# Optimization experiments

Hardware: AMD Instinct MI355X
Metric: run time of the kernel (lower is better)

## Reference

```python
import jax, jax.numpy as jnp
import numpy as np

CAMS, HEADS, PTS, LAYERS = 6, 8, 2, 3
D, DH, FFN = 256, 32, 512
VZ, VH, VW = 8, 50, 50
NQ = VZ * VH * VW
IN_C = 768
IMG_H, IMG_W = 256, 704
FH, FW = IMG_H // 32, IMG_W // 32   # 8, 22
L = FH * FW                         # 176 tokens per camera
LVIS = 44                           # visible tokens (mask_ratio=0.75)


def _layer_norm(x, g, b, eps=1e-5):
    m = x.mean(-1, keepdims=True)
    v = x.var(-1, keepdims=True)
    return (x - m) / jnp.sqrt(v + eps) * g + b


def _group_norm(x, g, b, groups=16, eps=1e-5):
    B, C = x.shape[0], x.shape[1]
    xg = x.reshape(B, groups, C // groups, *x.shape[2:])
    m = xg.mean(axis=(2, 3, 4, 5), keepdims=True)
    v = xg.var(axis=(2, 3, 4, 5), keepdims=True)
    xg = (xg - m) / jnp.sqrt(v + eps)
    return xg.reshape(x.shape) * g[None, :, None, None, None] + b[None, :, None, None, None]


def _bilinear(val, loc, Hf, Wf):
    # val: [C, HW, heads, dh]; loc: [C, NQ, heads, P, 2] as (x, y) pixel coords
    x, y = loc[..., 0], loc[..., 1]
    x0 = jnp.floor(x); y0 = jnp.floor(y)
    wx, wy = x - x0, y - y0
    x0i, y0i = x0.astype(jnp.int32), y0.astype(jnp.int32)
    cidx = jnp.arange(val.shape[0])[:, None, None, None]
    hidx = jnp.arange(val.shape[2])[None, None, :, None]

    def g(yi, xi):
        idx = jnp.clip(yi, 0, Hf - 1) * Wf + jnp.clip(xi, 0, Wf - 1)
        return val[cidx, idx, hidx]  # [C,NQ,heads,P,dh]

    out = ((1 - wx) * (1 - wy))[..., None] * g(y0i, x0i)
    out = out + (wx * (1 - wy))[..., None] * g(y0i, x0i + 1)
    out = out + ((1 - wx) * wy)[..., None] * g(y0i + 1, x0i)
    out = out + (wx * wy)[..., None] * g(y0i + 1, x0i + 1)
    return out


def setup_inputs() -> dict:
    key = jax.random.key(0)
    ks = iter(jax.random.split(key, 48))

    def rn(shape, s=0.02):
        return jax.random.normal(next(ks), shape, jnp.float32) * s

    return {
        'camera_x': jax.random.normal(next(ks), (CAMS, LVIS, IN_C), jnp.float32),
        'camera_ids_restore': jax.random.randint(next(ks), (CAMS, L), 0, L),
        'img_h': IMG_H, 'img_w': IMG_W,
        'mask_token': rn((1, 1, IN_C)),
        'vol_emb': rn((NQ, D), 1.0),
        'W_tc': rn((D, IN_C)), 'b_tc': jnp.zeros((D,), jnp.float32),
        'cams_embeds': rn((CAMS, D), 1.0),
        'level_embeds': rn((1, D), 1.0),
        'W_off': rn((LAYERS, D, HEADS * CAMS * PTS * 2)),
        'b_off': rn((LAYERS, HEADS * CAMS * PTS * 2), 2.0),
        'W_att': rn((LAYERS, D, HEADS * CAMS * PTS)),
        'b_att': jnp.zeros((LAYERS, HEADS * CAMS * PTS), jnp.float32),
        'W_val': rn((LAYERS, D, D)), 'b_val': jnp.zeros((LAYERS, D), jnp.float32),
        'W_out': rn((LAYERS, D, D)), 'b_out': jnp.zeros((LAYERS, D), jnp.float32),
        'ln1_g': jnp.ones((LAYERS, D), jnp.float32), 'ln1_b': jnp.zeros((LAYERS, D), jnp.float32),
        'W_ff1': rn((LAYERS, D, FFN)), 'b_ff1': jnp.zeros((LAYERS, FFN), jnp.float32),
        'W_ff2': rn((LAYERS, FFN, D)), 'b_ff2': jnp.zeros((LAYERS, D), jnp.float32),
        'ln2_g': jnp.ones((LAYERS, D), jnp.float32), 'ln2_b': jnp.zeros((LAYERS, D), jnp.float32),
        'deconv_w': rn((D, D, 2, 2, 2)),
        'gn1_g': jnp.ones((D,), jnp.float32), 'gn1_b': jnp.zeros((D,), jnp.float32),
        'conv3_w': rn((192, D, 3, 3, 3)),
        'gn2_g': jnp.ones((192,), jnp.float32), 'gn2_b': jnp.zeros((192,), jnp.float32),
    }


def _forward(camera_x, camera_ids_restore, img_h, img_w, mask_token, vol_emb, W_tc, b_tc,
             cams_embeds, level_embeds, W_off, b_off, W_att, b_att, W_val, b_val, W_out, b_out,
             ln1_g, ln1_b, W_ff1, b_ff1, W_ff2, b_ff2, ln2_g, ln2_b,
             deconv_w, gn1_g, gn1_b, conv3_w, gn2_g, gn2_b):
    N, Lfull = camera_ids_restore.shape
    # 1) MAE unshuffle: append mask tokens, gather back to original order
    mt = jnp.broadcast_to(mask_token, (N, Lfull - camera_x.shape[1], IN_C)).astype(camera_x.dtype)
    full = jnp.concatenate([camera_x, mt], axis=1)                         # [N,L,C]
    full = jnp.take_along_axis(full, camera_ids_restore[:, :, None], axis=1)
    Hf, Wf = img_h // 32, img_w // 32
    cam_x = jnp.transpose(full, (0, 2, 1)).reshape(1, N, IN_C, Hf, Wf)     # [1,6,768,8,22]
    # 2) 1x1 transfer conv + ReLU
    vf = jax.nn.relu(jnp.einsum('bnchw,oc->bnohw', cam_x, W_tc) + b_tc[None, None, :, None, None])
    # 3) flatten spatial + cam/level embeds -> per-camera feature maps [N,HW,D]
    vf = jnp.transpose(vf.reshape(1, N, D, Hf * Wf), (1, 0, 3, 2))          # [N,1,HW,D]
    vf = vf + cams_embeds[:, None, None, :] + level_embeds[None, None, 0:1, :]
    feat = vf[:, 0]                                                         # [N,HW,D]
    # 4) reference points of volume queries (z slow, h, w fast) -> pixel coords
    ww = (jnp.arange(VW, dtype=jnp.float32) + 0.5) / VW
    hh = (jnp.arange(VH, dtype=jnp.float32) + 0.5) / VH
    grid = jnp.stack([jnp.tile(ww, VH), jnp.repeat(hh, VW)], axis=-1)       # [VH*VW,2]
    ref_pix = jnp.tile(grid, (VZ, 1)) * jnp.array([Wf, Hf], jnp.float32) - 0.5  # [NQ,2]
    # 5) deformable cross-attention volume encoder
    q = vol_emb
    for l in range(LAYERS):
        off = (q @ W_off[l] + b_off[l]).reshape(NQ, HEADS, CAMS, PTS, 2)
        att = jax.nn.softmax((q @ W_att[l] + b_att[l]).reshape(NQ, HEADS, CAMS * PTS), axis=-1)
        att = jnp.transpose(att.reshape(NQ, HEADS, CAMS, PTS), (2, 0, 1, 3))      # [C,NQ,H,P]
        val = (feat @ W_val[l] + b_val[l]).reshape(CAMS, Hf * Wf, HEADS, DH)
        loc = jnp.transpose(ref_pix[:, None, None, None, :] + off, (2, 0, 1, 3, 4))  # [C,NQ,H,P,2]
        sampled = _bilinear(val, loc, Hf, Wf)                                     # [C,NQ,H,P,DH]
        agg = jnp.einsum('cnhp,cnhpd->nhd', att, sampled).reshape(NQ, D)
        q = _layer_norm(q + agg @ W_out[l] + b_out[l], ln1_g[l], ln1_b[l])
        q = _layer_norm(q + jax.nn.relu(q @ W_ff1[l] + b_ff1[l]) @ W_ff2[l] + b_ff2[l], ln2_g[l], ln2_b[l])
    # 6) reshape -> [1, D, VW, VH, VZ] (matches .permute(0,4,3,2,1))
    vol = jnp.transpose(q.reshape(1, VZ, VH, VW, D), (0, 4, 3, 2, 1))
    # 7) deblock: deconv3d(k=2,s=2) -> GN16 -> ReLU -> conv3d(k=3,p=1) -> GN16 -> ReLU
    x = jax.lax.conv_transpose(vol, deconv_w, (2, 2, 2), 'VALID',
                               dimension_numbers=('NCDHW', 'OIDHW', 'NCDHW'))
    x = jax.nn.relu(_group_norm(x, gn1_g, gn1_b))
    x = jax.lax.conv_general_dilated(x, conv3_w, (1, 1, 1), [(1, 1)] * 3,
                                     dimension_numbers=('NCDHW', 'OIDHW', 'NCDHW'))
    x = jax.nn.relu(_group_norm(x, gn2_g, gn2_b))
    return x, cam_x


def reference(camera_x, camera_ids_restore, img_h, img_w, mask_token, vol_emb, W_tc, b_tc,
              cams_embeds, level_embeds, W_off, b_off, W_att, b_att, W_val, b_val, W_out, b_out,
              ln1_g, ln1_b, W_ff1, b_ff1, W_ff2, b_ff2, ln2_g, ln2_b,
              deconv_w, gn1_g, gn1_b, conv3_w, gn2_g, gn2_b):
    return _forward(camera_x, camera_ids_restore, img_h, img_w, mask_token, vol_emb, W_tc, b_tc,
                    cams_embeds, level_embeds, W_off, b_off, W_att, b_att, W_val, b_val, W_out, b_out,
                    ln1_g, ln1_b, W_ff1, b_ff1, W_ff2, b_ff2, ln2_g, ln2_b,
                    deconv_w, gn1_g, gn1_b, conv3_w, gn2_g, gn2_b)
```

## Files before the change

### kernel.cpp

```cpp
#include <hip/hip_runtime.h>
#include <stdint.h>

typedef __attribute__((ext_vector_type(8))) short s16x8;
typedef __attribute__((ext_vector_type(4))) float f32x4;

static __device__ __forceinline__ unsigned short f2bf(float f) {
  unsigned u = __float_as_uint(f);
  u += 0x7FFFu + ((u >> 16) & 1u);
  return (unsigned short)(u >> 16);
}
static __device__ __forceinline__ float bf2f(unsigned short h) {
  return __uint_as_float(((unsigned)h) << 16);
}
static __device__ __forceinline__ void sum8(uint4 u, float& a, float& q) {
  unsigned w[4] = {u.x, u.y, u.z, u.w};
#pragma unroll
  for (int i = 0; i < 4; ++i) {
    float v0 = __uint_as_float((w[i] & 0xFFFFu) << 16);
    float v1 = __uint_as_float(w[i] & 0xFFFF0000u);
    a += v0 + v1;
    q += v0 * v0 + v1 * v1;
  }
}

__global__ void k_wt(const float* __restrict__ in, unsigned short* __restrict__ out,
                     int K, int N, int outL, int total) {
  int idx = blockIdx.x * 256 + threadIdx.x;
  if (idx >= total) return;
  int kn = K * N;
  int l = idx / kn, r = idx - l * kn;
  int k = r / N, n = r - k * N;
  out[(size_t)l * outL + (size_t)n * K + k] = f2bf(in[idx]);
}

__global__ void k_wdc(const float* __restrict__ in, unsigned short* __restrict__ out) {
  int idx = blockIdx.x * 256 + threadIdx.x;
  int n = idx >> 8, k = idx & 255;
  out[idx] = f2bf(in[((size_t)(n & 255)) * 2048 + k * 8 + (n >> 8)]);
}

__global__ void k_wc3(const float* __restrict__ W, unsigned short* __restrict__ T) {
  int idx = blockIdx.x * 256 + threadIdx.x;
  int tap = idx / 49152;
  int rem = idx - tap * 49152;
  int oc = rem >> 8, ic = rem & 255;
  int chunk = ic >> 5, kg = (ic >> 3) & 3, j = ic & 7;
  int ocblk = oc >> 4, lo = oc & 15;
  size_t frag = (size_t)(tap * 8 + chunk) * 12 + ocblk;
  T[(frag * 64 + kg * 16 + lo) * 8 + j] = f2bf(W[(oc * 256 + ic) * 27 + tap]);
}

__global__ void k_cvt(const float* __restrict__ in, unsigned short* __restrict__ out, int n) {
  int i = blockIdx.x * 256 + threadIdx.x;
  if (i < n) out[i] = f2bf(in[i]);
}

__global__ void k_wtct(const float* __restrict__ W, float* __restrict__ T) {
  int idx = blockIdx.x * 256 + threadIdx.x;
  int k = idx >> 8, o = idx & 255;
  T[idx] = W[o * 768 + k];
}

__global__ void k_restore(const float* __restrict__ cx, const int* __restrict__ ids,
                          const float* __restrict__ mtok, float* __restrict__ out) {
  int idx = blockIdx.x * 256 + threadIdx.x;
  int p = idx % 176;
  int r = idx / 176;
  int ch = r % 768;
  int c = r / 768;
  int id = ids[c * 176 + p];
  out[idx] = (id < 44) ? cx[((size_t)(c * 44 + id)) * 768 + ch] : mtok[ch];
}

__global__ __launch_bounds__(256) void k_vf(const float* __restrict__ camx, const float* __restrict__ WtT,
                                            const float* __restrict__ btc, const float* __restrict__ cemb,
                                            const float* __restrict__ lemb, unsigned short* __restrict__ featb) {
  __shared__ float sa[768];
  int blk = blockIdx.x;
  int c = blk / 176, p = blk - c * 176;
  int t = threadIdx.x;
  for (int i = t; i < 768; i += 256) sa[i] = camx[((size_t)(c * 768 + i)) * 176 + p];
  __syncthreads();
  float acc = 0.f;
  for (int k = 0; k < 768; ++k) acc += sa[k] * WtT[k * 256 + t];
  featb[(size_t)blk * 256 + t] = f2bf(fmaxf(acc + btc[t], 0.f) + cemb[c * 256 + t] + lemb[t]);
}

__global__ __launch_bounds__(256) void k_gemm(
    const unsigned short* __restrict__ A, int M, int lda,
    const unsigned short* __restrict__ Bt, int K, int N,
    const float* __restrict__ bias, const float* __restrict__ bias2, int n1, int relu,
    float* __restrict__ Cf, unsigned short* __restrict__ Cb, int ldc, int mode) {
  __shared__ short sA[128 * 40];
  const int t = threadIdx.x;
  const int l = t & 63, w = t >> 6;
  const int lo = l & 15, kg = l >> 4;
  const int row0 = blockIdx.x * 128, n0 = blockIdx.y * 64;
  const s16x8 bz = {0, 0, 0, 0, 0, 0, 0, 0};
  f32x4 acc[2][4] = {};
  s16x8 bc[4], bn[4];
#pragma unroll
  for (int nb = 0; nb < 4; ++nb) {
    int n = n0 + nb * 16 + lo;
    bc[nb] = (n < N) ? *(const s16x8*)&Bt[(size_t)n * K + kg * 8] : bz;
  }
  const int stR = t >> 1, stH = t & 1;
  for (int kc = 0; kc < K; kc += 32) {
    const bool pf = (kc + 32 < K);
    if (pf) {
#pragma unroll
      for (int nb = 0; nb < 4; ++nb) {
        int n = n0 + nb * 16 + lo;
        bn[nb] = (n < N) ? *(const s16x8*)&Bt[(size_t)n * K + kc + 32 + kg * 8] : bz;
      }
    }
    __syncthreads();
    {
      int r = row0 + stR;
// ... 21 lines not shown
  }
#pragma unroll
  for (int m = 0; m < 2; ++m)
#pragma unroll
    for (int nb = 0; nb < 4; ++nb)
#pragma unroll
      for (int r = 0; r < 4; ++r) {
        int row = row0 + w * 32 + m * 16 + (kg << 2) + r;
        int col = n0 + nb * 16 + lo;
        if (row < M && col < N) {
          float v = acc[m][nb][r];
          if (bias) v += (col < n1) ? bias[col] : bias2[col - n1];
          if (relu) v = fmaxf(v, 0.f);
          if (mode == 0) {
            Cf[(size_t)row * ldc + col] = v;
          } else if (mode == 2) {
            Cb[(size_t)row * ldc + col] = f2bf(v);
          } else {
            int tap = col >> 8, oc = col & 255;
            int z = row / 2500, rr = row - z * 2500;
            int hy = rr / 50, wx = rr - hy * 50;
            int t1 = tap >> 2, t2 = (tap >> 1) & 1, t3 = tap & 1;
            int od = 2 * wx + 1 - t1, oh = 2 * hy + 1 - t2, ow = 2 * z + 1 - t3;
            Cb[((size_t)((od * 100 + oh) * 16 + ow)) * 256 + oc] = f2bf(v);
          }
        }
      }
}

__global__ __launch_bounds__(256) void k_sample(const float* __restrict__ oa,
                                                const float* __restrict__ val,
                                                unsigned short* __restrict__ aggb) {
  __shared__ float sl[96], sw[96];
  int n = blockIdx.x, t = threadIdx.x;
  if (t < 96) sl[t] = oa[(size_t)n * 288 + 192 + t];
  __syncthreads();
  if (t < 8) {
    float mx = -1e30f;
    for (int j = 0; j < 12; ++j) mx = fmaxf(mx, sl[t * 12 + j]);
    float s = 0.f;
    for (int j = 0; j < 12; ++j) s += __expf(sl[t * 12 + j] - mx);
    float inv = 1.f / s;
    for (int j = 0; j < 12; ++j) sw[t * 12 + j] = __expf(sl[t * 12 + j] - mx) * inv;
  }
  __syncthreads();
  int h = t >> 5, d = t & 31;
  float xr = ((float)(n % 50) + 0.5f) * (22.0f / 50.0f) - 0.5f;
  float yr = ((float)((n / 50) % 50) + 0.5f) * (8.0f / 50.0f) - 0.5f;
  float acc = 0.f;
  const float* offn = oa + (size_t)n * 288 + h * 24;
  const float* vbh = val + (size_t)h * 32 + d;
#pragma unroll
  for (int c = 0; c < 6; ++c)
#pragma unroll
    for (int p2 = 0; p2 < 2; ++p2) {
      float x = xr + offn[(c * 2 + p2) * 2];
      float y = yr + offn[(c * 2 + p2) * 2 + 1];
      float x0 = floorf(x), y0 = floorf(y);
      float wx = x - x0, wy = y - y0;
      int ix0 = min(max((int)x0, 0), 21), ix1 = min(max((int)x0 + 1, 0), 21);
      int iy0 = min(max((int)y0, 0), 7), iy1 = min(max((int)y0 + 1, 0), 7);
      const float* vb = vbh + (size_t)c * 176 * 256;
      float v00 = vb[(size_t)(iy0 * 22 + ix0) * 256];
      float v01 = vb[(size_t)(iy0 * 22 + ix1) * 256];
      float v10 = vb[(size_t)(iy1 * 22 + ix0) * 256];
      float v11 = vb[(size_t)(iy1 * 22 + ix1) * 256];
      float bil = (1.f - wx) * (1.f - wy) * v00 + wx * (1.f - wy) * v01 +
                  (1.f - wx) * wy * v10 + wx * wy * v11;
      acc += sw[h * 12 + c * 2 + p2] * bil;
    }
  aggb[(size_t)n * 256 + t] = f2bf(acc);
}

__global__ __launch_bounds__(256) void k_addln(float* __restrict__ q, const float* __restrict__ p,
                                               const float* __restrict__ g, const float* __restrict__ b,
                                               unsigned short* __restrict__ qb) {
  __shared__ float red[8];
  int n = blockIdx.x, t = threadIdx.x;
  float x = q[(size_t)n * 256 + t] + p[(size_t)n * 256 + t];
  float s1 = x, s2 = x * x;
#pragma unroll
  for (int o = 32; o >= 1; o >>= 1) {
    s1 += __shfl_xor(s1, o, 64);
    s2 += __shfl_xor(s2, o, 64);
  }
  int w = t >> 6;
  if ((t & 63) == 0) { red[w * 2] = s1; red[w * 2 + 1] = s2; }
  __syncthreads();
  s1 = red[0] + red[2] + red[4] + red[6];
  s2 = red[1] + red[3] + red[5] + red[7];
  float mean = s1 * (1.0f / 256.0f);
  float var = s2 * (1.0f / 256.0f) - mean * mean;
  float y = (x - mean) * rsqrtf(var + 1e-5f) * g[t] + b[t];
  q[(size_t)n * 256 + t] = y;
  qb[(size_t)n * 256 + t] = f2bf(y);
}

__global__ __launch_bounds__(256) void k_gnstat1(const unsigned short* __restrict__ X, float* __restrict__ part) {
  __shared__ float s1[256], s2[256];
  int b = blockIdx.x, t = threadIdx.x;
  int oc8 = t & 31, v0 = t >> 5;
  float a = 0.f, q = 0.f;
#pragma unroll
  for (int i = 0; i < 8; ++i) {
    int vox = v0 + i * 8;
    uint4 u = *(const uint4*)&X[(size_t)b * 16384 + vox * 256 + oc8 * 8];
    sum8(u, a, q);
  }
  s1[t] = a; s2[t] = q;
  __syncthreads();
  if (t < 128) { s1[t] += s1[t + 128]; s2[t] += s2[t + 128]; }
  __syncthreads();
  if (t < 64) { s1[t] += s1[t + 64]; s2[t] += s2[t + 64]; }
  __syncthreads();
  if (t < 32) { s1[t] += s1[t + 32]; s2[t] += s2[t + 32]; }
  __syncthreads();
  if (t < 16) {
    part[t * 2500 + b] = s1[2 * t] + s1[2 * t + 1];
    part[40000 + t * 2500 + b] = s2[2 * t] + s2[2 * t + 1];
  }
}

__global__ __launch_bounds__(256) void k_gnred1(const float* __restrict__ part, float* __restrict__ gmv) {
  __shared__ float s1[256], s2[256];
  int g = blockIdx.x, t = threadIdx.x;
  float a = 0.f, q = 0.f;
  for (int i = t; i < 2500; i += 256) { a += part[g * 2500 + i]; q += part[40000 + g * 2500 + i]; }
  s1[t] = a; s2[t] = q;
  __syncthreads();
  for (int s = 128; s > 0; s >>= 1) {
    if (t < s) { s1[t] += s1[t + s]; s2[t] += s2[t + s]; }
    __syncthreads();
  }
  if (t == 0) {
    float m = s1[0] / 2560000.0f;
    float v = s2[0] / 2560000.0f - m * m;
    gmv[2 * g] = m; gmv[2 * g + 1] = rsqrtf(v + 1e-5f);
  }
}

__global__ __launch_bounds__(256) void k_gnapply1(unsigned short* __restrict__ X, const float* __restrict__ gmv,
                                                  const float* __restrict__ g, const float* __restrict__ b) {
  for (unsigned i = blockIdx.x * 256 + threadIdx.x; i < 5120000u; i += gridDim.x * 256) {
    unsigned e = i * 8u;
    int oc0 = e & 255, grp = oc0 >> 4;
    float mean = gmv[grp * 2], rstd = gmv[grp * 2 + 1];
    float4 g0 = *(const float4*)&g[oc0], g1 = *(const float4*)&g[oc0 + 4];
    float4 b0 = *(const float4*)&b[oc0], b1 = *(const float4*)&b[oc0 + 4];
    uint4 u = *(const uint4*)&X[e];
    unsigned w[4] = {u.x, u.y, u.z, u.w};
    float gg[8] = {g0.x, g0.y, g0.z, g0.w, g1.x, g1.y, g1.z, g1.w};
    float bb[8] = {b0.x, b0.y, b0.z, b0.w, b1.x, b1.y, b1.z, b1.w};
    unsigned o[4];
#pragma unroll
    for (int j = 0; j < 4; ++j) {
      float v0 = __uint_as_float((w[j] & 0xFFFFu) << 16);
      float v1 = __uint_as_float(w[j] & 0xFFFF0000u);
      v0 = fmaxf((v0 - mean) * rstd * gg[2 * j] + bb[2 * j], 0.f);
      v1 = fmaxf((v1 - mean) * rstd * gg[2 * j + 1] + bb[2 * j + 1], 0.f);
      o[j] = (unsigned)f2bf(v0) | ((unsigned)f2bf(v1) << 16);
    }
    *(uint4*)&X[e] = make_uint4(o[0], o[1], o[2], o[3]);
  }
}

__global__ __launch_bounds__(256, 2) void k_conv3(const unsigned short* __restrict__ X,
                                                  const unsigned short* __restrict__ Wp,
                                                  unsigned short* __restrict__ Y) {
  __shared__ short sX[4 * 543 * 8];
  int bid = blockIdx.x;
  int xcd = bid & 7, idx = bid >> 3;
  int swz = (xcd < 4 ? xcd * 163 : 652 + (xcd - 4) * 162) + idx;
  const int od = swz / 13;
  const int oh0 = (swz - od * 13) * 8;
  const int t = threadIdx.x;
  const int l = t & 63, w = t >> 6;
  const int kg = l >> 4, lo = l & 15;
  f32x4 acc[8][3] = {};
  s16x8 bc[9], bn[9];
  const unsigned short* Wl = Wp + (size_t)l * 8;
  const int w3 = w * 3;
#pragma unroll
  for (int t2 = 0; t2 < 3; ++t2)
#pragma unroll
    for (int nb = 0; nb < 3; ++nb)
      bc[t2 * 3 + nb] = *(const s16x8*)&Wl[(size_t)((t2 * 3 * 8) * 12 + w3 + nb) * 512];

  for (int g = 0; g < 72; ++g) {
    const int chunk = g / 9;
    const int sub = g - chunk * 9;
    const int t1 = sub / 3, t3 = sub - t1 * 3;
    if (sub == 0) {
      __syncthreads();
#pragma unroll
      for (int i = 0; i < 9; ++i) {
        int e = t + i * 256;
        if (e < 2160) {
          int pos = e >> 2, ks = e & 3;
          int sd = pos / 180, r2 = pos - sd * 180;
          int sh = r2 / 18, sw_ = r2 - sh * 18;
          int gd = od + sd - 1, gh = oh0 + sh - 1, gw = sw_ - 1;
          uint4 v = {0u, 0u, 0u, 0u};
          if ((unsigned)gd < 100u && (unsigned)gh < 100u && (unsigned)gw < 16u)
            v = *(const uint4*)&X[((size_t)((gd * 100 + gh) * 16 + gw)) * 256 + chunk * 32 + ks * 8];
          *(uint4*)&sX[(ks * 543 + pos) * 8] = v;
        }
      }
      __syncthreads();
    }
    const int g1 = g + 1;
    if (g1 < 72) {
      const int c1 = g1 / 9, s1 = g1 - c1 * 9;
      const int t1n = s1 / 3, t3n = s1 - t1n * 3;
#pragma unroll
      for (int t2 = 0; t2 < 3; ++t2)
#pragma unroll
        for (int nb = 0; nb < 3; ++nb)
          bn[t2 * 3 + nb] = *(const s16x8*)&Wl[
              (size_t)(((t1n * 9 + t2 * 3 + t3n) * 8 + c1) * 12 + w3 + nb) * 512];
    }
    const int abase = kg * 543 + t1 * 180 + lo + t3;
#pragma unroll
    for (int sh = 0; sh < 10; ++sh) {
      s16x8 a = *(const s16x8*)&sX[(abase + sh * 18) * 8];
#pragma unroll
      for (int t2 = 0; t2 < 3; ++t2) {
        const int m = sh - t2;
        if (m >= 0 && m < 8) {
          acc[m][0] = __builtin_amdgcn_mfma_f32_16x16x32_bf16(a, bc[t2 * 3 + 0], acc[m][0], 0, 0, 0);
          acc[m][1] = __builtin_amdgcn_mfma_f32_16x16x32_bf16(a, bc[t2 * 3 + 1], acc[m][1], 0, 0, 0);
          acc[m][2] = __builtin_amdgcn_mfma_f32_16x16x32_bf16(a, bc[t2 * 3 + 2], acc[m][2], 0, 0, 0);
        }
      }
    }
#pragma unroll
    for (int i = 0; i < 9; ++i) bc[i] = bn[i];
  }
#pragma unroll
  for (int m = 0; m < 8; ++m) {
    int oh = oh0 + m;
    if (oh < 100) {
#pragma unroll
      for (int nb = 0; nb < 3; ++nb)
#pragma unroll
        for (int r = 0; r < 4; ++r) {
          int oc = w * 48 + nb * 16 + lo;
          int ow = (kg << 2) + r;
          Y[(size_t)oc * 160000 + (size_t)((od * 100 + oh) * 16) + ow] = f2bf(acc[m][nb][r]);
        }
    }
  }
}

__global__ __launch_bounds__(256) void k_gnstat2(const unsigned short* __restrict__ X, float* __restrict__ part) {
  __shared__ float s1[256], s2[256];
  int b = blockIdx.x, t = threadIdx.x;
  int ch = b / 10, pp = b - ch * 10;
  const unsigned short* base = X + (size_t)ch * 160000 + (size_t)pp * 16000;
  float a = 0.f, q = 0.f;
  for (int i = t; i < 2000; i += 256) {
    uint4 u = *(const uint4*)&base[i * 8];
    sum8(u, a, q);
  }
  s1[t] = a; s2[t] = q;
  __syncthreads();
  for (int s = 128; s > 0; s >>= 1) {
    if (t < s) { s1[t] += s1[t + s]; s2[t] += s2[t + s]; }
    __syncthreads();
  }
  if (t == 0) { part[80000 + ch * 10 + pp] = s1[0]; part[81920 + ch * 10 + pp] = s2[0]; }
}

__global__ __launch_bounds__(256) void k_gnred2(const float* __restrict__ part, float* __restrict__ gmv) {
  __shared__ float s1[256], s2[256];
  int g = blockIdx.x, t = threadIdx.x;
  float a = (t < 120) ? part[80000 + g * 120 + t] : 0.f;
  float q = (t < 120) ? part[81920 + g * 120 + t] : 0.f;
  s1[t] = a; s2[t] = q;
  __syncthreads();
// ... 59 lines not shown
  const float* b_ff1 = (const float*)d_in[21];
  const float* W_ff2 = (const float*)d_in[22];
  const float* b_ff2 = (const float*)d_in[23];
  const float* ln2_g = (const float*)d_in[24];
  const float* ln2_b = (const float*)d_in[25];
  const float* deconv_w = (const float*)d_in[26];
  const float* gn1_g = (const float*)d_in[27];
  const float* gn1_b = (const float*)d_in[28];
  const float* conv3_w = (const float*)d_in[29];
  const float* gn2_g = (const float*)d_in[30];
  const float* gn2_b = (const float*)d_in[31];

  char* ws = (char*)d_ws;
  float* q             = (float*)(ws + 0);
  unsigned short* qb   = (unsigned short*)(ws + 20480000);
  float* proj          = (float*)(ws + 30720000);
  float* oa            = (float*)(ws + 51200000);
  unsigned short* aggb = (unsigned short*)(ws + 74240000);
  unsigned short* ffhb = (unsigned short*)(ws + 84480000);
  float* val           = (float*)(ws + 104960000);
  unsigned short* featb= (unsigned short*)(ws + 106041344);
  unsigned short* x1bf = (unsigned short*)(ws + 30720000);
  unsigned short* c3   = (unsigned short*)(ws + 112640000);
  unsigned short* Wt_val = (unsigned short*)(ws + 174080000);
  unsigned short* Wt_oa  = (unsigned short*)(ws + 174473216);
  unsigned short* Wt_out = (unsigned short*)(ws + 174915584);
  unsigned short* Wt_ff1 = (unsigned short*)(ws + 175308800);
  unsigned short* Wt_ff2 = (unsigned short*)(ws + 176095232);
  unsigned short* Wt_dc  = (unsigned short*)(ws + 176881664);
  unsigned short* wc3    = (unsigned short*)(ws + 177930240);
  float* part = (float*)(ws + 180584448);
  float* gmv1 = (float*)(ws + 180920320);
  float* gmv2 = (float*)(ws + 180920448);
  float* wtcT = (float*)(ws + 180920576);

  float* out_x = (float*)d_out;
  float* out_camx = out_x + 30720000;

  k_wtct<<<768, 256, 0, stream>>>(W_tc, wtcT);
  k_wt<<<(3 * 65536 + 255) / 256, 256, 0, stream>>>(W_val, Wt_val, 256, 256, 65536, 3 * 65536);
  k_wt<<<(3 * 49152 + 255) / 256, 256, 0, stream>>>(W_off, Wt_oa, 256, 192, 73728, 3 * 49152);
  k_wt<<<(3 * 24576 + 255) / 256, 256, 0, stream>>>(W_att, Wt_oa + 192 * 256, 256, 96, 73728, 3 * 24576);
  k_wt<<<(3 * 65536 + 255) / 256, 256, 0, stream>>>(W_out, Wt_out, 256, 256, 65536, 3 * 65536);
  k_wt<<<(3 * 131072 + 255) / 256, 256, 0, stream>>>(W_ff1, Wt_ff1, 256, 512, 131072, 3 * 131072);
  k_wt<<<(3 * 131072 + 255) / 256, 256, 0, stream>>>(W_ff2, Wt_ff2, 512, 256, 131072, 3 * 131072);
  k_wdc<<<2048, 256, 0, stream>>>(deconv_w, Wt_dc);
  k_wc3<<<5184, 256, 0, stream>>>(conv3_w, wc3);

  k_restore<<<3168, 256, 0, stream>>>(camera_x, ids, mask_tok, out_camx);
  k_vf<<<1056, 256, 0, stream>>>(out_camx, wtcT, b_tc, cams_emb, lvl_emb, featb);
  hipMemcpyAsync(q, vol_emb, (size_t)20000 * 256 * 4, hipMemcpyDeviceToDevice, stream);
  k_cvt<<<20000, 256, 0, stream>>>(vol_emb, qb, 5120000);

  for (int lyr = 0; lyr < 3; ++lyr) {
    k_gemm<<<gemm_grid(1056, 256), 256, 0, stream>>>(featb, 1056, 256, Wt_val + lyr * 65536, 256, 256,
                                                     b_val + lyr * 256, nullptr, 256, 0, val, nullptr, 256, 0);
    k_gemm<<<gemm_grid(20000, 288), 256, 0, stream>>>(qb, 20000, 256, Wt_oa + lyr * 73728, 256, 288,
                                                      b_off + lyr * 192, b_att + lyr * 96, 192, 0,
                                                      oa, nullptr, 288, 0);
    k_sample<<<20000, 256, 0, stream>>>(oa, val, aggb);
    k_gemm<<<gemm_grid(20000, 256), 256, 0, stream>>>(aggb, 20000, 256, Wt_out + lyr * 65536, 256, 256,
                                                      b_out + lyr * 256, nullptr, 256, 0, proj, nullptr, 256, 0);
    k_addln<<<20000, 256, 0, stream>>>(q, proj, ln1_g + lyr * 256, ln1_b + lyr * 256, qb);
    k_gemm<<<gemm_grid(20000, 512), 256, 0, stream>>>(qb, 20000, 256, Wt_ff1 + lyr * 131072, 256, 512,
                                                      b_ff1 + lyr * 512, nullptr, 512, 1, nullptr, ffhb, 512, 2);
    k_gemm<<<gemm_grid(20000, 256), 256, 0, stream>>>(ffhb, 20000, 512, Wt_ff2 + lyr * 131072, 512, 256,
                                                      b_ff2 + lyr * 256, nullptr, 256, 0, proj, nullptr, 256, 0);
    k_addln<<<20000, 256, 0, stream>>>(q, proj, ln2_g + lyr * 256, ln2_b + lyr * 256, qb);
  }

  k_gemm<<<gemm_grid(20000, 2048), 256, 0, stream>>>(qb, 20000, 256, Wt_dc, 256, 2048,
                                                     nullptr, nullptr, 2048, 0, nullptr, x1bf, 256, 1);

  k_gnstat1<<<2500, 256, 0, stream>>>(x1bf, part);
  k_gnred1<<<16, 256, 0, stream>>>(part, gmv1);
  k_gnapply1<<<2048, 256, 0, stream>>>(x1bf, gmv1, gn1_g, gn1_b);

  k_conv3<<<1300, 256, 0, stream>>>(x1bf, wc3, c3);

  k_gnstat2<<<1920, 256, 0, stream>>>(c3, part);
  k_gnred2<<<16, 256, 0, stream>>>(part, gmv2);
  k_gnapply2<<<2048, 256, 0, stream>>>(c3, gmv2, gn2_g, gn2_b, out_x);
}
```

Measured before the change: 1.353 ms.

## Fuse GroupNorm1 apply into conv3 load, rebalance conv3 waves, batch rows in sample/addln

The GN1 normalize+ReLU pass is folded into the conv3 shared-memory staging, using per-channel scale and shift precomputed by a tiny kernel. This removes one full read-modify-write pass over the 80 MB bf16 volume. conv3 moves from 4 to 6 waves per block, each owning 32 output channels instead of 48, with fewer live registers, occupancy hint 3, and s_setprio around the MFMA loop. k_sample and k_addln each process 8 rows per block to cut launch and block overhead, at the cost of extra barriers and less parallelism per block.

```diff
diff --git a/kernel.cpp b/kernel.cpp
--- a/kernel.cpp
+++ b/kernel.cpp
@@ -171,68 +171,77 @@
                                                 const float* __restrict__ val,
                                                 unsigned short* __restrict__ aggb) {
   __shared__ float sl[96], sw[96];
-  int n = blockIdx.x, t = threadIdx.x;
-  if (t < 96) sl[t] = oa[(size_t)n * 288 + 192 + t];
-  __syncthreads();
-  if (t < 8) {
-    float mx = -1e30f;
-    for (int j = 0; j < 12; ++j) mx = fmaxf(mx, sl[t * 12 + j]);
-    float s = 0.f;
-    for (int j = 0; j < 12; ++j) s += __expf(sl[t * 12 + j] - mx);
-    float inv = 1.f / s;
-    for (int j = 0; j < 12; ++j) sw[t * 12 + j] = __expf(sl[t * 12 + j] - mx) * inv;
-  }
-  __syncthreads();
+  int t = threadIdx.x;
   int h = t >> 5, d = t & 31;
-  float xr = ((float)(n % 50) + 0.5f) * (22.0f / 50.0f) - 0.5f;
-  float yr = ((float)((n / 50) % 50) + 0.5f) * (8.0f / 50.0f) - 0.5f;
-  float acc = 0.f;
-  const float* offn = oa + (size_t)n * 288 + h * 24;
-  const float* vbh = val + (size_t)h * 32 + d;
-#pragma unroll
-  for (int c = 0; c < 6; ++c)
-#pragma unroll
-    for (int p2 = 0; p2 < 2; ++p2) {
-      float x = xr + offn[(c * 2 + p2) * 2];
-      float y = yr + offn[(c * 2 + p2) * 2 + 1];
-      float x0 = floorf(x), y0 = floorf(y);
-      float wx = x - x0, wy = y - y0;
-      int ix0 = min(max((int)x0, 0), 21), ix1 = min(max((int)x0 + 1, 0), 21);
-      int iy0 = min(max((int)y0, 0), 7), iy1 = min(max((int)y0 + 1, 0), 7);
-      const float* vb = vbh + (size_t)c * 176 * 256;
-      float v00 = vb[(size_t)(iy0 * 22 + ix0) * 256];
-      float v01 = vb[(size_t)(iy0 * 22 + ix1) * 256];
-      float v10 = vb[(size_t)(iy1 * 22 + ix0) * 256];
-      float v11 = vb[(size_t)(iy1 * 22 + ix1) * 256];
-      float bil = (1.f - wx) * (1.f - wy) * v00 + wx * (1.f - wy) * v01 +
-                  (1.f - wx) * wy * v10 + wx * wy * v11;
-      acc += sw[h * 12 + c * 2 + p2] * bil;
-    }
-  aggb[(size_t)n * 256 + t] = f2bf(acc);
+  const float* vbh0 = val + (size_t)h * 32 + d;
+  for (int r = 0; r < 8; ++r) {
+    int n = blockIdx.x * 8 + r;
+    if (t < 96) sl[t] = oa[(size_t)n * 288 + 192 + t];
+    __syncthreads();
+    if (t < 8) {
+      float mx = -1e30f;
+      for (int j = 0; j < 12; ++j) mx = fmaxf(mx, sl[t * 12 + j]);
+      float s = 0.f;
+      for (int j = 0; j < 12; ++j) s += __expf(sl[t * 12 + j] - mx);
+      float inv = 1.f / s;
+      for (int j = 0; j < 12; ++j) sw[t * 12 + j] = __expf(sl[t * 12 + j] - mx) * inv;
+    }
+    __syncthreads();
+    float xr = ((float)(n % 50) + 0.5f) * (22.0f / 50.0f) - 0.5f;
+    float yr = ((float)((n / 50) % 50) + 0.5f) * (8.0f / 50.0f) - 0.5f;
+    float acc = 0.f;
+    const float* offn = oa + (size_t)n * 288 + h * 24;
+#pragma unroll
+    for (int c = 0; c < 6; ++c)
+#pragma unroll
+      for (int p2 = 0; p2 < 2; ++p2) {
+        float x = xr + offn[(c * 2 + p2) * 2];
+        float y = yr + offn[(c * 2 + p2) * 2 + 1];
+        float x0 = floorf(x), y0 = floorf(y);
+        float wx = x - x0, wy = y - y0;
+        int ix0 = min(max((int)x0, 0), 21), ix1 = min(max((int)x0 + 1, 0), 21);
+        int iy0 = min(max((int)y0, 0), 7), iy1 = min(max((int)y0 + 1, 0), 7);
+        const float* vb = vbh0 + (size_t)c * 176 * 256;
+        float v00 = vb[(size_t)(iy0 * 22 + ix0) * 256];
+        float v01 = vb[(size_t)(iy0 * 22 + ix1) * 256];
+        float v10 = vb[(size_t)(iy1 * 22 + ix0) * 256];
+        float v11 = vb[(size_t)(iy1 * 22 + ix1) * 256];
+        float bil = (1.f - wx) * (1.f - wy) * v00 + wx * (1.f - wy) * v01 +
+                    (1.f - wx) * wy * v10 + wx * wy * v11;
+        acc += sw[h * 12 + c * 2 + p2] * bil;
+      }
+    aggb[(size_t)n * 256 + t] = f2bf(acc);
+    __syncthreads();
+  }
 }
 
 __global__ __launch_bounds__(256) void k_addln(float* __restrict__ q, const float* __restrict__ p,
                                                const float* __restrict__ g, const float* __restrict__ b,
                                                unsigned short* __restrict__ qb) {
   __shared__ float red[8];
-  int n = blockIdx.x, t = threadIdx.x;
-  float x = q[(size_t)n * 256 + t] + p[(size_t)n * 256 + t];
-  float s1 = x, s2 = x * x;
-#pragma unroll
-  for (int o = 32; o >= 1; o >>= 1) {
-    s1 += __shfl_xor(s1, o, 64);
-    s2 += __shfl_xor(s2, o, 64);
-  }
+  int t = threadIdx.x;
   int w = t >> 6;
-  if ((t & 63) == 0) { red[w * 2] = s1; red[w * 2 + 1] = s2; }
-  __syncthreads();
-  s1 = red[0] + red[2] + red[4] + red[6];
-  s2 = red[1] + red[3] + red[5] + red[7];
-  float mean = s1 * (1.0f / 256.0f);
-  float var = s2 * (1.0f / 256.0f) - mean * mean;
-  float y = (x - mean) * rsqrtf(var + 1e-5f) * g[t] + b[t];
-  q[(size_t)n * 256 + t] = y;
-  qb[(size_t)n * 256 + t] = f2bf(y);
+  float gg = g[t], bb = b[t];
+  for (int r = 0; r < 8; ++r) {
+    size_t n = (size_t)blockIdx.x * 8 + r;
+    float x = q[n * 256 + t] + p[n * 256 + t];
+    float s1 = x, s2 = x * x;
+#pragma unroll
+    for (int o = 32; o >= 1; o >>= 1) {
+      s1 += __shfl_xor(s1, o, 64);
+      s2 += __shfl_xor(s2, o, 64);
+    }
+    if ((t & 63) == 0) { red[w * 2] = s1; red[w * 2 + 1] = s2; }
+    __syncthreads();
+    s1 = red[0] + red[2] + red[4] + red[6];
+    s2 = red[1] + red[3] + red[5] + red[7];
+    float mean = s1 * (1.0f / 256.0f);
+    float var = s2 * (1.0f / 256.0f) - mean * mean;
+    float y = (x - mean) * rsqrtf(var + 1e-5f) * gg + bb;
+    q[n * 256 + t] = y;
+    qb[n * 256 + t] = f2bf(y);
+    __syncthreads();
+  }
 }
 
 __global__ __launch_bounds__(256) void k_gnstat1(const unsigned short* __restrict__ X, float* __restrict__ part) {
@@ -278,33 +287,19 @@
   }
 }
 
-__global__ __launch_bounds__(256) void k_gnapply1(unsigned short* __restrict__ X, const float* __restrict__ gmv,
-                                                  const float* __restrict__ g, const float* __restrict__ b) {
-  for (unsigned i = blockIdx.x * 256 + threadIdx.x; i < 5120000u; i += gridDim.x * 256) {
-    unsigned e = i * 8u;
-    int oc0 = e & 255, grp = oc0 >> 4;
-    float mean = gmv[grp * 2], rstd = gmv[grp * 2 + 1];
-    float4 g0 = *(const float4*)&g[oc0], g1 = *(const float4*)&g[oc0 + 4];
-    float4 b0 = *(const float4*)&b[oc0], b1 = *(const float4*)&b[oc0 + 4];
-    uint4 u = *(const uint4*)&X[e];
-    unsigned w[4] = {u.x, u.y, u.z, u.w};
-    float gg[8] = {g0.x, g0.y, g0.z, g0.w, g1.x, g1.y, g1.z, g1.w};
-    float bb[8] = {b0.x, b0.y, b0.z, b0.w, b1.x, b1.y, b1.z, b1.w};
-    unsigned o[4];
-#pragma unroll
-    for (int j = 0; j < 4; ++j) {
-      float v0 = __uint_as_float((w[j] & 0xFFFFu) << 16);
-      float v1 = __uint_as_float(w[j] & 0xFFFF0000u);
-      v0 = fmaxf((v0 - mean) * rstd * gg[2 * j] + bb[2 * j], 0.f);
-      v1 = fmaxf((v1 - mean) * rstd * gg[2 * j + 1] + bb[2 * j + 1], 0.f);
-      o[j] = (unsigned)f2bf(v0) | ((unsigned)f2bf(v1) << 16);
-    }
-    *(uint4*)&X[e] = make_uint4(o[0], o[1], o[2], o[3]);
-  }
-}
-
-__global__ __launch_bounds__(256, 2) void k_conv3(const unsigned short* __restrict__ X,
+__global__ void k_gnscale(const float* __restrict__ gmv, const float* __restrict__ g,
+                          const float* __restrict__ b, float* __restrict__ sct) {
+  int t = threadIdx.x;
+  int grp = t >> 4;
+  float mean = gmv[2 * grp], rstd = gmv[2 * grp + 1];
+  float s = rstd * g[t];
+  sct[t] = s;
+  sct[256 + t] = b[t] - mean * s;
+}
+
+__global__ __launch_bounds__(384, 3) void k_conv3(const unsigned short* __restrict__ X,
                                                   const unsigned short* __restrict__ Wp,
+                                                  const float* __restrict__ sct,
                                                   unsigned short* __restrict__ Y) {
   __shared__ short sX[4 * 543 * 8];
   int bid = blockIdx.x;
@@ -315,50 +310,70 @@
   const int t = threadIdx.x;
   const int l = t & 63, w = t >> 6;
   const int kg = l >> 4, lo = l & 15;
-  f32x4 acc[8][3] = {};
-  s16x8 bc[9], bn[9];
+  f32x4 acc[8][2] = {};
+  s16x8 bc[6], bn[6];
   const unsigned short* Wl = Wp + (size_t)l * 8;
-  const int w3 = w * 3;
+  const int w2 = w * 2;
 #pragma unroll
   for (int t2 = 0; t2 < 3; ++t2)
 #pragma unroll
-    for (int nb = 0; nb < 3; ++nb)
-      bc[t2 * 3 + nb] = *(const s16x8*)&Wl[(size_t)((t2 * 3 * 8) * 12 + w3 + nb) * 512];
-
-  for (int g = 0; g < 72; ++g) {
-    const int chunk = g / 9;
-    const int sub = g - chunk * 9;
+    for (int nb = 0; nb < 2; ++nb)
+      bc[t2 * 2 + nb] = *(const s16x8*)&Wl[(size_t)((t2 * 3 * 8) * 12 + w2 + nb) * 512];
+
+  for (int gi = 0; gi < 72; ++gi) {
+    const int chunk = gi / 9;
+    const int sub = gi - chunk * 9;
     const int t1 = sub / 3, t3 = sub - t1 * 3;
     if (sub == 0) {
       __syncthreads();
 #pragma unroll
-      for (int i = 0; i < 9; ++i) {
-        int e = t + i * 256;
+      for (int i = 0; i < 6; ++i) {
+        int e = t + i * 384;
         if (e < 2160) {
           int pos = e >> 2, ks = e & 3;
           int sd = pos / 180, r2 = pos - sd * 180;
           int sh = r2 / 18, sw_ = r2 - sh * 18;
           int gd = od + sd - 1, gh = oh0 + sh - 1, gw = sw_ - 1;
           uint4 v = {0u, 0u, 0u, 0u};
-          if ((unsigned)gd < 100u && (unsigned)gh < 100u && (unsigned)gw < 16u)
+          if ((unsigned)gd < 100u && (unsigned)gh < 100u && (unsigned)gw < 16u) {
             v = *(const uint4*)&X[((size_t)((gd * 100 + gh) * 16 + gw)) * 256 + chunk * 32 + ks * 8];
+            int ic0 = chunk * 32 + ks * 8;
+            float4 sA0 = *(const float4*)&sct[ic0];
+            float4 sA1 = *(const float4*)&sct[ic0 + 4];
+            float4 tA0 = *(const float4*)&sct[256 + ic0];
+            float4 tA1 = *(const float4*)&sct[256 + ic0 + 4];
+            float sc[8] = {sA0.x, sA0.y, sA0.z, sA0.w, sA1.x, sA1.y, sA1.z, sA1.w};
+            float tt[8] = {tA0.x, tA0.y, tA0.z, tA0.w, tA1.x, tA1.y, tA1.z, tA1.w};
+            unsigned wv[4] = {v.x, v.y, v.z, v.w};
+            unsigned o[4];
+#pragma unroll
+            for (int j = 0; j < 4; ++j) {
+              float v0 = __uint_as_float((wv[j] & 0xFFFFu) << 16);
+              float v1 = __uint_as_float(wv[j] & 0xFFFF0000u);
+              v0 = fmaxf(v0 * sc[2 * j] + tt[2 * j], 0.f);
+              v1 = fmaxf(v1 * sc[2 * j + 1] + tt[2 * j + 1], 0.f);
+              o[j] = (unsigned)f2bf(v0) | ((unsigned)f2bf(v1) << 16);
+            }
+            v = make_uint4(o[0], o[1], o[2], o[3]);
+          }
           *(uint4*)&sX[(ks * 543 + pos) * 8] = v;
         }
       }
       __syncthreads();
     }
-    const int g1 = g + 1;
-    if (g1 < 72) {
-      const int c1 = g1 / 9, s1 = g1 - c1 * 9;
-      const int t1n = s1 / 3, t3n = s1 - t1n * 3;
+    const int gn1 = gi + 1;
+    if (gn1 < 72) {
+      const int c1 = gn1 / 9, su1 = gn1 - c1 * 9;
+      const int t1n = su1 / 3, t3n = su1 - t1n * 3;
 #pragma unroll
       for (int t2 = 0; t2 < 3; ++t2)
 #pragma unroll
-        for (int nb = 0; nb < 3; ++nb)
-          bn[t2 * 3 + nb] = *(const s16x8*)&Wl[
-              (size_t)(((t1n * 9 + t2 * 3 + t3n) * 8 + c1) * 12 + w3 + nb) * 512];
+        for (int nb = 0; nb < 2; ++nb)
+          bn[t2 * 2 + nb] = *(const s16x8*)&Wl[
+              (size_t)(((t1n * 9 + t2 * 3 + t3n) * 8 + c1) * 12 + w2 + nb) * 512];
     }
     const int abase = kg * 543 + t1 * 180 + lo + t3;
+    __builtin_amdgcn_s_setprio(1);
 #pragma unroll
     for (int sh = 0; sh < 10; ++sh) {
       s16x8 a = *(const s16x8*)&sX[(abase + sh * 18) * 8];
@@ -366,24 +381,24 @@
       for (int t2 = 0; t2 < 3; ++t2) {
         const int m = sh - t2;
         if (m >= 0 && m < 8) {
-          acc[m][0] = __builtin_amdgcn_mfma_f32_16x16x32_bf16(a, bc[t2 * 3 + 0], acc[m][0], 0, 0, 0);
-          acc[m][1] = __builtin_amdgcn_mfma_f32_16x16x32_bf16(a, bc[t2 * 3 + 1], acc[m][1], 0, 0, 0);
-          acc[m][2] = __builtin_amdgcn_mfma_f32_16x16x32_bf16(a, bc[t2 * 3 + 2], acc[m][2], 0, 0, 0);
+          acc[m][0] = __builtin_amdgcn_mfma_f32_16x16x32_bf16(a, bc[t2 * 2 + 0], acc[m][0], 0, 0, 0);
+          acc[m][1] = __builtin_amdgcn_mfma_f32_16x16x32_bf16(a, bc[t2 * 2 + 1], acc[m][1], 0, 0, 0);
         }
       }
     }
-#pragma unroll
-    for (int i = 0; i < 9; ++i) bc[i] = bn[i];
+    __builtin_amdgcn_s_setprio(0);
+#pragma unroll
+    for (int i = 0; i < 6; ++i) bc[i] = bn[i];
   }
 #pragma unroll
   for (int m = 0; m < 8; ++m) {
     int oh = oh0 + m;
     if (oh < 100) {
 #pragma unroll
-      for (int nb = 0; nb < 3; ++nb)
+      for (int nb = 0; nb < 2; ++nb)
 #pragma unroll
         for (int r = 0; r < 4; ++r) {
-          int oc = w * 48 + nb * 16 + lo;
+          int oc = w * 32 + nb * 16 + lo;
           int ow = (kg << 2) + r;
           Y[(size_t)oc * 160000 + (size_t)((od * 100 + oh) * 16) + ow] = f2bf(acc[m][nb][r]);
         }
@@ -510,6 +525,7 @@
   float* gmv1 = (float*)(ws + 180920320);
   float* gmv2 = (float*)(ws + 180920448);
   float* wtcT = (float*)(ws + 180920576);
+  float* sct  = (float*)(ws + 181707008);
 
   float* out_x = (float*)d_out;
   float* out_camx = out_x + 30720000;
@@ -535,15 +551,15 @@
     k_gemm<<<gemm_grid(20000, 288), 256, 0, stream>>>(qb, 20000, 256, Wt_oa + lyr * 73728, 256, 288,
                                                       b_off + lyr * 192, b_att + lyr * 96, 192, 0,
                                                       oa, nullptr, 288, 0);
-    k_sample<<<20000, 256, 0, stream>>>(oa, val, aggb);
+    k_sample<<<2500, 256, 0, stream>>>(oa, val, aggb);
     k_gemm<<<gemm_grid(20000, 256), 256, 0, stream>>>(aggb, 20000, 256, Wt_out + lyr * 65536, 256, 256,
                                                       b_out + lyr * 256, nullptr, 256, 0, proj, nullptr, 256, 0);
-    k_addln<<<20000, 256, 0, stream>>>(q, proj, ln1_g + lyr * 256, ln1_b + lyr * 256, qb);
+    k_addln<<<2500, 256, 0, stream>>>(q, proj, ln1_g + lyr * 256, ln1_b + lyr * 256, qb);
     k_gemm<<<gemm_grid(20000, 512), 256, 0, stream>>>(qb, 20000, 256, Wt_ff1 + lyr * 131072, 256, 512,
                                                       b_ff1 + lyr * 512, nullptr, 512, 1, nullptr, ffhb, 512, 2);
     k_gemm<<<gemm_grid(20000, 256), 256, 0, stream>>>(ffhb, 20000, 512, Wt_ff2 + lyr * 131072, 512, 256,
                                                       b_ff2 + lyr * 256, nullptr, 256, 0, proj, nullptr, 256, 0);
-    k_addln<<<20000, 256, 0, stream>>>(q, proj, ln2_g + lyr * 256, ln2_b + lyr * 256, qb);
+    k_addln<<<2500, 256, 0, stream>>>(q, proj, ln2_g + lyr * 256, ln2_b + lyr * 256, qb);
   }
 
   k_gemm<<<gemm_grid(20000, 2048), 256, 0, stream>>>(qb, 20000, 256, Wt_dc, 256, 2048,
@@ -551,9 +567,9 @@
 
   k_gnstat1<<<2500, 256, 0, stream>>>(x1bf, part);
   k_gnred1<<<16, 256, 0, stream>>>(part, gmv1);
-  k_gnapply1<<<2048, 256, 0, stream>>>(x1bf, gmv1, gn1_g, gn1_b);
-
-  k_conv3<<<1300, 256, 0, stream>>>(x1bf, wc3, c3);
+  k_gnscale<<<1, 256, 0, stream>>>(gmv1, gn1_g, gn1_b, sct);
+
+  k_conv3<<<1300, 384, 0, stream>>>(x1bf, wc3, sct, c3);
 
   k_gnstat2<<<1920, 256, 0, stream>>>(c3, part);
   k_gnred2<<<16, 256, 0, stream>>>(part, gmv2);
```

Result: slower. 1.549 ms (+14.5%).

## Route camera projection through MFMA GEMM and batch rows in sample/LN kernels

Applied to the files above, without the earlier changes.

The scalar fp32 camera-token projection kernel is replaced by a bf16 restore-transpose, a call to the existing MFMA GEMM with bias and ReLU, and a separate embedding-add pass. The sampling and add-LayerNorm kernels now process 8 rows per block with 2500 blocks instead of 20000, which cuts launch and block-scheduling overhead. The sampling softmax is also parallelised across 96 threads. The projection input is now bf16 and the embeddings are added after a bf16 rounding, which adds rounding error. Fewer blocks may also reduce the latency hiding available for the gathers.

```diff
diff --git a/kernel.cpp b/kernel.cpp
--- a/kernel.cpp
+++ b/kernel.cpp
@@ -55,12 +55,6 @@
   if (i < n) out[i] = f2bf(in[i]);
 }
 
-__global__ void k_wtct(const float* __restrict__ W, float* __restrict__ T) {
-  int idx = blockIdx.x * 256 + threadIdx.x;
-  int k = idx >> 8, o = idx & 255;
-  T[idx] = W[o * 768 + k];
-}
-
 __global__ void k_restore(const float* __restrict__ cx, const int* __restrict__ ids,
                           const float* __restrict__ mtok, float* __restrict__ out) {
   int idx = blockIdx.x * 256 + threadIdx.x;
@@ -72,18 +66,23 @@
   out[idx] = (id < 44) ? cx[((size_t)(c * 44 + id)) * 768 + ch] : mtok[ch];
 }
 
-__global__ __launch_bounds__(256) void k_vf(const float* __restrict__ camx, const float* __restrict__ WtT,
-                                            const float* __restrict__ btc, const float* __restrict__ cemb,
-                                            const float* __restrict__ lemb, unsigned short* __restrict__ featb) {
-  __shared__ float sa[768];
-  int blk = blockIdx.x;
-  int c = blk / 176, p = blk - c * 176;
-  int t = threadIdx.x;
-  for (int i = t; i < 768; i += 256) sa[i] = camx[((size_t)(c * 768 + i)) * 176 + p];
-  __syncthreads();
-  float acc = 0.f;
-  for (int k = 0; k < 768; ++k) acc += sa[k] * WtT[k * 256 + t];
-  featb[(size_t)blk * 256 + t] = f2bf(fmaxf(acc + btc[t], 0.f) + cemb[c * 256 + t] + lemb[t]);
+__global__ void k_restoreT(const float* __restrict__ cx, const int* __restrict__ ids,
+                           const float* __restrict__ mtok, unsigned short* __restrict__ out) {
+  int idx = blockIdx.x * 256 + threadIdx.x;
+  int ch = idx % 768;
+  int row = idx / 768;
+  int c = row / 176, p = row - c * 176;
+  int id = ids[c * 176 + p];
+  float v = (id < 44) ? cx[((size_t)(c * 44 + id)) * 768 + ch] : mtok[ch];
+  out[idx] = f2bf(v);
+}
+
+__global__ void k_embadd(unsigned short* __restrict__ featb, const float* __restrict__ cemb,
+                         const float* __restrict__ lemb) {
+  int idx = blockIdx.x * 256 + threadIdx.x;
+  int col = idx & 255;
+  int c = idx / (176 * 256);
+  featb[idx] = f2bf(bf2f(featb[idx]) + cemb[c * 256 + col] + lemb[col]);
 }
 
 __global__ __launch_bounds__(256) void k_gemm(
@@ -171,68 +170,80 @@
                                                 const float* __restrict__ val,
                                                 unsigned short* __restrict__ aggb) {
   __shared__ float sl[96], sw[96];
-  int n = blockIdx.x, t = threadIdx.x;
-  if (t < 96) sl[t] = oa[(size_t)n * 288 + 192 + t];
-  __syncthreads();
-  if (t < 8) {
-    float mx = -1e30f;
-    for (int j = 0; j < 12; ++j) mx = fmaxf(mx, sl[t * 12 + j]);
-    float s = 0.f;
-    for (int j = 0; j < 12; ++j) s += __expf(sl[t * 12 + j] - mx);
-    float inv = 1.f / s;
-    for (int j = 0; j < 12; ++j) sw[t * 12 + j] = __expf(sl[t * 12 + j] - mx) * inv;
-  }
-  __syncthreads();
+  int t = threadIdx.x;
   int h = t >> 5, d = t & 31;
-  float xr = ((float)(n % 50) + 0.5f) * (22.0f / 50.0f) - 0.5f;
-  float yr = ((float)((n / 50) % 50) + 0.5f) * (8.0f / 50.0f) - 0.5f;
-  float acc = 0.f;
-  const float* offn = oa + (size_t)n * 288 + h * 24;
-  const float* vbh = val + (size_t)h * 32 + d;
-#pragma unroll
-  for (int c = 0; c < 6; ++c)
-#pragma unroll
-    for (int p2 = 0; p2 < 2; ++p2) {
-      float x = xr + offn[(c * 2 + p2) * 2];
-      float y = yr + offn[(c * 2 + p2) * 2 + 1];
-      float x0 = floorf(x), y0 = floorf(y);
-      float wx = x - x0, wy = y - y0;
-      int ix0 = min(max((int)x0, 0), 21), ix1 = min(max((int)x0 + 1, 0), 21);
-      int iy0 = min(max((int)y0, 0), 7), iy1 = min(max((int)y0 + 1, 0), 7);
-      const float* vb = vbh + (size_t)c * 176 * 256;
-      float v00 = vb[(size_t)(iy0 * 22 + ix0) * 256];
-      float v01 = vb[(size_t)(iy0 * 22 + ix1) * 256];
-      float v10 = vb[(size_t)(iy1 * 22 + ix0) * 256];
-      float v11 = vb[(size_t)(iy1 * 22 + ix1) * 256];
-      float bil = (1.f - wx) * (1.f - wy) * v00 + wx * (1.f - wy) * v01 +
-                  (1.f - wx) * wy * v10 + wx * wy * v11;
-      acc += sw[h * 12 + c * 2 + p2] * bil;
-    }
-  aggb[(size_t)n * 256 + t] = f2bf(acc);
+  const float* vbh0 = val + (size_t)h * 32 + d;
+  for (int r = 0; r < 8; ++r) {
+    int n = blockIdx.x * 8 + r;
+    if (t < 96) sl[t] = oa[(size_t)n * 288 + 192 + t];
+    __syncthreads();
+    if (t < 96) {
+      int hh = t / 12;
+      float mx = -1e30f;
+#pragma unroll
+      for (int j = 0; j < 12; ++j) mx = fmaxf(mx, sl[hh * 12 + j]);
+      sw[t] = __expf(sl[t] - mx);
+    }
+    __syncthreads();
+    float ssum = 0.f;
+#pragma unroll
+    for (int j = 0; j < 12; ++j) ssum += sw[h * 12 + j];
+    float inv = 1.f / ssum;
+    float xr = ((float)(n % 50) + 0.5f) * (22.0f / 50.0f) - 0.5f;
+    float yr = ((float)((n / 50) % 50) + 0.5f) * (8.0f / 50.0f) - 0.5f;
+    float acc = 0.f;
+    const float* offn = oa + (size_t)n * 288 + h * 24;
+#pragma unroll
+    for (int c = 0; c < 6; ++c)
+#pragma unroll
+      for (int p2 = 0; p2 < 2; ++p2) {
+        float x = xr + offn[(c * 2 + p2) * 2];
+        float y = yr + offn[(c * 2 + p2) * 2 + 1];
+        float x0 = floorf(x), y0 = floorf(y);
+        float wx = x - x0, wy = y - y0;
+        int ix0 = min(max((int)x0, 0), 21), ix1 = min(max((int)x0 + 1, 0), 21);
+        int iy0 = min(max((int)y0, 0), 7), iy1 = min(max((int)y0 + 1, 0), 7);
+        const float* vb = vbh0 + (size_t)c * 176 * 256;
+        float v00 = vb[(size_t)(iy0 * 22 + ix0) * 256];
+        float v01 = vb[(size_t)(iy0 * 22 + ix1) * 256];
+        float v10 = vb[(size_t)(iy1 * 22 + ix0) * 256];
+        float v11 = vb[(size_t)(iy1 * 22 + ix1) * 256];
+        float bil = (1.f - wx) * (1.f - wy) * v00 + wx * (1.f - wy) * v01 +
+                    (1.f - wx) * wy * v10 + wx * wy * v11;
+        acc += sw[h * 12 + c * 2 + p2] * inv * bil;
+      }
+    aggb[(size_t)n * 256 + t] = f2bf(acc);
+    __syncthreads();
+  }
 }
 
 __global__ __launch_bounds__(256) void k_addln(float* __restrict__ q, const float* __restrict__ p,
                                                const float* __restrict__ g, const float* __restrict__ b,
                                                unsigned short* __restrict__ qb) {
   __shared__ float red[8];
-  int n = blockIdx.x, t = threadIdx.x;
-  float x = q[(size_t)n * 256 + t] + p[(size_t)n * 256 + t];
-  float s1 = x, s2 = x * x;
-#pragma unroll
-  for (int o = 32; o >= 1; o >>= 1) {
-    s1 += __shfl_xor(s1, o, 64);
-    s2 += __shfl_xor(s2, o, 64);
-  }
+  int t = threadIdx.x;
   int w = t >> 6;
-  if ((t & 63) == 0) { red[w * 2] = s1; red[w * 2 + 1] = s2; }
-  __syncthreads();
-  s1 = red[0] + red[2] + red[4] + red[6];
-  s2 = red[1] + red[3] + red[5] + red[7];
-  float mean = s1 * (1.0f / 256.0f);
-  float var = s2 * (1.0f / 256.0f) - mean * mean;
-  float y = (x - mean) * rsqrtf(var + 1e-5f) * g[t] + b[t];
-  q[(size_t)n * 256 + t] = y;
-  qb[(size_t)n * 256 + t] = f2bf(y);
+  float gg = g[t], bb = b[t];
+  for (int r = 0; r < 8; ++r) {
+    size_t n = (size_t)blockIdx.x * 8 + r;
+    float x = q[n * 256 + t] + p[n * 256 + t];
+    float s1 = x, s2 = x * x;
+#pragma unroll
+    for (int o = 32; o >= 1; o >>= 1) {
+      s1 += __shfl_xor(s1, o, 64);
+      s2 += __shfl_xor(s2, o, 64);
+    }
+    if ((t & 63) == 0) { red[w * 2] = s1; red[w * 2 + 1] = s2; }
+    __syncthreads();
+    s1 = red[0] + red[2] + red[4] + red[6];
+    s2 = red[1] + red[3] + red[5] + red[7];
+    float mean = s1 * (1.0f / 256.0f);
+    float var = s2 * (1.0f / 256.0f) - mean * mean;
+    float y = (x - mean) * rsqrtf(var + 1e-5f) * gg + bb;
+    q[n * 256 + t] = y;
+    qb[n * 256 + t] = f2bf(y);
+    __syncthreads();
+  }
 }
 
 __global__ __launch_bounds__(256) void k_gnstat1(const unsigned short* __restrict__ X, float* __restrict__ part) {
@@ -325,9 +336,9 @@
     for (int nb = 0; nb < 3; ++nb)
       bc[t2 * 3 + nb] = *(const s16x8*)&Wl[(size_t)((t2 * 3 * 8) * 12 + w3 + nb) * 512];
 
-  for (int g = 0; g < 72; ++g) {
-    const int chunk = g / 9;
-    const int sub = g - chunk * 9;
+  for (int gi = 0; gi < 72; ++gi) {
+    const int chunk = gi / 9;
+    const int sub = gi - chunk * 9;
     const int t1 = sub / 3, t3 = sub - t1 * 3;
     if (sub == 0) {
       __syncthreads();
@@ -347,10 +358,10 @@
       }
       __syncthreads();
     }
-    const int g1 = g + 1;
-    if (g1 < 72) {
-      const int c1 = g1 / 9, s1 = g1 - c1 * 9;
-      const int t1n = s1 / 3, t3n = s1 - t1n * 3;
+    const int gn1 = gi + 1;
+    if (gn1 < 72) {
+      const int c1 = gn1 / 9, su1 = gn1 - c1 * 9;
+      const int t1n = su1 / 3, t3n = su1 - t1n * 3;
 #pragma unroll
       for (int t2 = 0; t2 < 3; ++t2)
 #pragma unroll
@@ -509,12 +520,13 @@
   float* part = (float*)(ws + 180584448);
   float* gmv1 = (float*)(ws + 180920320);
   float* gmv2 = (float*)(ws + 180920448);
-  float* wtcT = (float*)(ws + 180920576);
+  unsigned short* Wt_tc  = (unsigned short*)(ws + 180920576);
+  unsigned short* camxT  = (unsigned short*)(ws + 181707008);
 
   float* out_x = (float*)d_out;
   float* out_camx = out_x + 30720000;
 
-  k_wtct<<<768, 256, 0, stream>>>(W_tc, wtcT);
+  k_cvt<<<768, 256, 0, stream>>>(W_tc, Wt_tc, 196608);
   k_wt<<<(3 * 65536 + 255) / 256, 256, 0, stream>>>(W_val, Wt_val, 256, 256, 65536, 3 * 65536);
   k_wt<<<(3 * 49152 + 255) / 256, 256, 0, stream>>>(W_off, Wt_oa, 256, 192, 73728, 3 * 49152);
   k_wt<<<(3 * 24576 + 255) / 256, 256, 0, stream>>>(W_att, Wt_oa + 192 * 256, 256, 96, 73728, 3 * 24576);
@@ -525,7 +537,11 @@
   k_wc3<<<5184, 256, 0, stream>>>(conv3_w, wc3);
 
   k_restore<<<3168, 256, 0, stream>>>(camera_x, ids, mask_tok, out_camx);
-  k_vf<<<1056, 256, 0, stream>>>(out_camx, wtcT, b_tc, cams_emb, lvl_emb, featb);
+  k_restoreT<<<3168, 256, 0, stream>>>(camera_x, ids, mask_tok, camxT);
+  k_gemm<<<gemm_grid(1056, 256), 256, 0, stream>>>(camxT, 1056, 768, Wt_tc, 768, 256,
+                                                   b_tc, nullptr, 256, 1, nullptr, featb, 256, 2);
+  k_embadd<<<1056, 256, 0, stream>>>(featb, cams_emb, lvl_emb);
+
   hipMemcpyAsync(q, vol_emb, (size_t)20000 * 256 * 4, hipMemcpyDeviceToDevice, stream);
   k_cvt<<<20000, 256, 0, stream>>>(vol_emb, qb, 5120000);
 
@@ -535,15 +551,15 @@
     k_gemm<<<gemm_grid(20000, 288), 256, 0, stream>>>(qb, 20000, 256, Wt_oa + lyr * 73728, 256, 288,
                                                       b_off + lyr * 192, b_att + lyr * 96, 192, 0,
                                                       oa, nullptr, 288, 0);
-    k_sample<<<20000, 256, 0, stream>>>(oa, val, aggb);
+    k_sample<<<2500, 256, 0, stream>>>(oa, val, aggb);
     k_gemm<<<gemm_grid(20000, 256), 256, 0, stream>>>(aggb, 20000, 256, Wt_out + lyr * 65536, 256, 256,
                                                       b_out + lyr * 256, nullptr, 256, 0, proj, nullptr, 256, 0);
-    k_addln<<<20000, 256, 0, stream>>>(q, proj, ln1_g + lyr * 256, ln1_b + lyr * 256, qb);
+    k_addln<<<2500, 256, 0, stream>>>(q, proj, ln1_g + lyr * 256, ln1_b + lyr * 256, qb);
     k_gemm<<<gemm_grid(20000, 512), 256, 0, stream>>>(qb, 20000, 256, Wt_ff1 + lyr * 131072, 256, 512,
                                                       b_ff1 + lyr * 512, nullptr, 512, 1, nullptr, ffhb, 512, 2);
     k_gemm<<<gemm_grid(20000, 256), 256, 0, stream>>>(ffhb, 20000, 512, Wt_ff2 + lyr * 131072, 512, 256,
                                                       b_ff2 + lyr * 256, nullptr, 256, 0, proj, nullptr, 256, 0);
-    k_addln<<<20000, 256, 0, stream>>>(q, proj, ln2_g + lyr * 256, ln2_b + lyr * 256, qb);
+    k_addln<<<2500, 256, 0, stream>>>(q, proj, ln2_g + lyr * 256, ln2_b + lyr * 256, qb);
   }
 
   k_gemm<<<gemm_grid(20000, 2048), 256, 0, stream>>>(qb, 20000, 256, Wt_dc, 256, 2048,
```

After: 1.449 ms. +7.1%, slower.
